# Kernel optimization log

Measured on AMD Instinct MI355X. Metric: run time of the kernel, lower is better.

Reference implementation:

```python
import jax, jax.numpy as jnp
import numpy as np

N, E, B = 10000, 100000, 64
IN_DIM, EDGE_DIM = 16, 8
HID = [32, 64]
OUT_DIM = 128
BN_EPS = 1e-5


def setup_inputs() -> dict:
    key = jax.random.key(0)
    ks = iter(jax.random.split(key, 32))
    inp = {}
    inp["x"] = jax.random.normal(next(ks), (N, IN_DIM), dtype=jnp.float32)
    inp["edge_index"] = jax.random.randint(next(ks), (2, E), 0, N, dtype=jnp.int64)
    inp["edge_attr"] = jax.random.normal(next(ks), (E, EDGE_DIM), dtype=jnp.float32)
    inp["batch"] = jnp.sort(jax.random.randint(next(ks), (N,), 0, B, dtype=jnp.int64))
    inp["edge_batch"] = jax.random.randint(next(ks), (E,), 0, B, dtype=jnp.int64)
    pre = IN_DIM
    for i, hd in enumerate(HID):
        s = 1.0 / np.sqrt(EDGE_DIM)
        inp[f"w_nn{i}"] = jax.random.uniform(next(ks), (pre * hd, EDGE_DIM), jnp.float32, -s, s)
        inp[f"b_nn{i}"] = jax.random.uniform(next(ks), (pre * hd,), jnp.float32, -s, s)
        inp[f"root{i}"] = jax.random.normal(next(ks), (pre, hd), dtype=jnp.float32) / np.sqrt(pre)
        inp[f"bias{i}"] = jnp.zeros((hd,), dtype=jnp.float32)
        inp[f"gamma{i}"] = jnp.ones((hd,), dtype=jnp.float32)
        inp[f"beta{i}"] = jnp.zeros((hd,), dtype=jnp.float32)
        pre = hd
    s = 1.0 / np.sqrt(pre)
    inp["s_w"] = jax.random.uniform(next(ks), (OUT_DIM, pre), jnp.float32, -s, s)
    inp["s_b"] = jax.random.uniform(next(ks), (OUT_DIM,), jnp.float32, -s, s)
    inp["t_w"] = jax.random.uniform(next(ks), (OUT_DIM, pre), jnp.float32, -s, s)
    inp["t_b"] = jax.random.uniform(next(ks), (OUT_DIM,), jnp.float32, -s, s)
    return inp


def _nnconv(x, edge_index, edge_attr, w_nn, b_nn, root, bias, out_dim):
    src, dst = edge_index[0], edge_index[1]
    # per-edge weight matrices [E, in_dim, out_dim]
    W = (edge_attr @ w_nn.T + b_nn).reshape(edge_attr.shape[0], -1, out_dim)
    msg = jnp.einsum('ei,eio->eo', x[src], W)  # gather + per-edge matmul
    agg = jax.ops.segment_sum(msg, dst, num_segments=N)  # scatter-add
    return agg + x @ root + bias


def _bn(x, gamma, beta):
    mu = jnp.mean(x, axis=0)
    var = jnp.mean((x - mu) ** 2, axis=0)  # biased var (torch BN training)
    return gamma * (x - mu) * jax.lax.rsqrt(var + BN_EPS) + beta


def reference(x, edge_index, edge_attr, batch, edge_batch,
              w_nn0, b_nn0, root0, bias0, gamma0, beta0,
              w_nn1, b_nn1, root1, bias1, gamma1, beta1,
              s_w, s_b, t_w, t_b):
    x = jax.nn.relu(_bn(_nnconv(x, edge_index, edge_attr, w_nn0, b_nn0, root0, bias0, HID[0]), gamma0, beta0))
    x = jax.nn.relu(_bn(_nnconv(x, edge_index, edge_attr, w_nn1, b_nn1, root1, bias1, HID[1]), gamma1, beta1))
    s_x = jnp.clip(x @ s_w.T + s_b, -30.0, 30.0)
    t_x = x @ t_w.T + t_b
    f_x = jax.nn.sigmoid(-s_x) * jnp.tanh(t_x)  # 1/(1+exp(s)) == sigmoid(-s)
    return jax.ops.segment_sum(f_x, batch, num_segments=B)
```

## Files before the change

### kernel.cpp

```cpp
#include <hip/hip_runtime.h>
#include <math.h>

#define NN 10000
#define NE 100000
#define BN_EPS 1e-5f


__device__ __forceinline__ unsigned short f2bf(float f) {
  unsigned int u = __float_as_uint(f);
  u += 0x7FFF + ((u >> 16) & 1);
  return (unsigned short)(u >> 16);
}
__device__ __forceinline__ float bf2f(unsigned short h) {
  return __uint_as_float(((unsigned int)h) << 16);
}

__global__ __launch_bounds__(256) void k_prep(
    const float* __restrict__ w0, const float* __restrict__ b0,
    const float* __restrict__ root0,
    const float* __restrict__ w1, const float* __restrict__ b1,
    const float* __restrict__ root1,
    const float* __restrict__ s_w, const float* __restrict__ t_w,
    float* __restrict__ wT0, float* __restrict__ wT1, float* __restrict__ wstT,
    float* __restrict__ st0, float* __restrict__ st1, float* __restrict__ out)
{
  int gid = blockIdx.x * 256 + threadIdx.x;
  int gsz = gridDim.x * 256;
  for (int idx = gid; idx < 16 * 320; idx += gsz) {
    int i = idx / 320, c = idx - i * 320;
    float v;
    if (c < 256)      v = w0[(i * 32 + (c & 31)) * 8 + (c >> 5)];
    else if (c < 288) v = b0[i * 32 + (c - 256)];
    else              v = root0[i * 32 + (c - 288)];
    wT0[idx] = v;
  }
  for (int idx = gid; idx < 32 * 640; idx += gsz) {
    int i = idx / 640, c = idx - i * 640;
    float v;
    if (c < 512)      v = w1[(i * 64 + (c & 63)) * 8 + (c >> 6)];
    else if (c < 576) v = b1[i * 64 + (c - 512)];
    else              v = root1[i * 64 + (c - 576)];
    wT1[idx] = v;
  }
  for (int idx = gid; idx < 64 * 256; idx += gsz) {
    int i = idx >> 8, o = idx & 255;
    wstT[idx] = (o < 128) ? s_w[o * 64 + i] : t_w[(o - 128) * 64 + i];
  }
  for (int idx = gid; idx < 64 * 128; idx += gsz) out[idx] = 0.f;
  if (gid < 64)  st0[gid] = 0.f;
  if (gid < 128) st1[gid] = 0.f;
}

__global__ __launch_bounds__(320) void k_node0(
    const float* __restrict__ x, const float* __restrict__ wT0,
    const float* __restrict__ bias0,
    unsigned short* __restrict__ G0h, float* __restrict__ h0)
{
  int c = threadIdx.x;
  float wc[16];
#pragma unroll
  for (int i = 0; i < 16; ++i) wc[i] = wT0[i * 320 + c];
  float bi = (c >= 288) ? bias0[c - 288] : 0.f;

  int n0 = blockIdx.x * 20;
  for (int n = n0; n < n0 + 20; n += 2) {
    const float4* xa = (const float4*)(x + n * 16);
    float a0 = 0.f, a1 = 0.f;
#pragma unroll
    for (int q = 0; q < 4; ++q) {
      float4 v0 = xa[q], v1 = xa[q + 4];
      a0 = fmaf(v0.x, wc[4 * q + 0], a0); a1 = fmaf(v1.x, wc[4 * q + 0], a1);
      a0 = fmaf(v0.y, wc[4 * q + 1], a0); a1 = fmaf(v1.y, wc[4 * q + 1], a1);
      a0 = fmaf(v0.z, wc[4 * q + 2], a0); a1 = fmaf(v1.z, wc[4 * q + 2], a1);
      a0 = fmaf(v0.w, wc[4 * q + 3], a0); a1 = fmaf(v1.w, wc[4 * q + 3], a1);
    }
    if (c < 288) {
      G0h[n * 288 + c]       = f2bf(a0);
      G0h[(n + 1) * 288 + c] = f2bf(a1);
    } else {
      h0[n * 32 + (c - 288)]       = a0 + bi;
      h0[(n + 1) * 32 + (c - 288)] = a1 + bi;
    }
  }
}

__global__ __launch_bounds__(256) void k_edge0(
    const int* __restrict__ ei, const float* __restrict__ ea,
    const unsigned short* __restrict__ G0h, float* __restrict__ h0)
{
  int tid = threadIdx.x;
  int slot = tid >> 5;
  int o = tid & 31;
  int stride = gridDim.x * 8;
  for (int e = blockIdx.x * 8 + slot; e < NE; e += stride) {
    int src = ei[e], dst = ei[NE + e];
    const unsigned short* gr = G0h + src * 288;
    const float* er = ea + e * 8;
    float m = bf2f(gr[256 + o]);
#pragma unroll
    for (int k = 0; k < 8; ++k) m = fmaf(er[k], bf2f(gr[k * 32 + o]), m);
    unsafeAtomicAdd(&h0[dst * 32 + o], m);
  }
}

template <int C>
__global__ __launch_bounds__(256) void k_stats(
    const float* __restrict__ h, float* __restrict__ st)
{
  const int RPB = 256 / C;
  int tid = threadIdx.x;
  int col = tid % C, rg = tid / C;
  float s1 = 0.f, s2 = 0.f;
  int step = gridDim.x * RPB;
  for (int n = blockIdx.x * RPB + rg; n < NN; n += step) {
    float v = h[n * C + col];
    s1 += v; s2 += v * v;
  }
  __shared__ float l1[256], l2[256];
  l1[tid] = s1; l2[tid] = s2;
  __syncthreads();
  if (tid < C) {
    for (int r = 1; r < RPB; ++r) { s1 += l1[r * C + tid]; s2 += l2[r * C + tid]; }
    unsafeAtomicAdd(&st[tid], s1);
    unsafeAtomicAdd(&st[C + tid], s2);
  }
}

__global__ __launch_bounds__(256) void k_x1(
    float* __restrict__ h0, const float* __restrict__ st0,
    const float* __restrict__ g0, const float* __restrict__ be0)
{
  __shared__ float sc[32], sh[32];
  int tid = threadIdx.x;
  if (tid < 32) {
    float mu  = st0[tid] * (1.0f / NN);
    float var = st0[32 + tid] * (1.0f / NN) - mu * mu;
    float s   = g0[tid] * rsqrtf(var + BN_EPS);
    sc[tid] = s;
    sh[tid] = be0[tid] - mu * s;
  }
  __syncthreads();
  const int NV = NN * 8;
  for (int i = blockIdx.x * 256 + tid; i < NV; i += gridDim.x * 256) {
    float4 v = ((const float4*)h0)[i];
    int c0 = (i * 4) & 31;
    v.x = fmaxf(fmaf(v.x, sc[c0],     sh[c0]),     0.f);
    v.y = fmaxf(fmaf(v.y, sc[c0 + 1], sh[c0 + 1]), 0.f);
    v.z = fmaxf(fmaf(v.z, sc[c0 + 2], sh[c0 + 2]), 0.f);
    v.w = fmaxf(fmaf(v.w, sc[c0 + 3], sh[c0 + 3]), 0.f);
    ((float4*)h0)[i] = v;
  }
}

__global__ __launch_bounds__(320) void k_node1(
    const float* __restrict__ x1, const float* __restrict__ wT1,
    const float* __restrict__ bias1,
    unsigned short* __restrict__ G1h, float* __restrict__ h1)
{
  int t = threadIdx.x;
  float wa[32], wb[32];
#pragma unroll
  for (int i = 0; i < 32; ++i) {
    float2 w2 = *(const float2*)(wT1 + i * 640 + 2 * t);
    wa[i] = w2.x; wb[i] = w2.y;
  }
  float bia = 0.f, bib = 0.f;
  if (t >= 288) { bia = bias1[2 * (t - 288)]; bib = bias1[2 * (t - 288) + 1]; }

  int n0 = blockIdx.x * 20;
  for (int n = n0; n < n0 + 20; n += 2) {
    const float4* xa = (const float4*)(x1 + n * 32);
    float a00 = 0.f, a01 = 0.f, a10 = 0.f, a11 = 0.f;
#pragma unroll
    for (int q = 0; q < 8; ++q) {
      float4 v0 = xa[q], v1 = xa[q + 8];
      a00 = fmaf(v0.x, wa[4 * q + 0], a00); a01 = fmaf(v0.x, wb[4 * q + 0], a01);
      a00 = fmaf(v0.y, wa[4 * q + 1], a00); a01 = fmaf(v0.y, wb[4 * q + 1], a01);
      a00 = fmaf(v0.z, wa[4 * q + 2], a00); a01 = fmaf(v0.z, wb[4 * q + 2], a01);
      a00 = fmaf(v0.w, wa[4 * q + 3], a00); a01 = fmaf(v0.w, wb[4 * q + 3], a01);
      a10 = fmaf(v1.x, wa[4 * q + 0], a10); a11 = fmaf(v1.x, wb[4 * q + 0], a11);
      a10 = fmaf(v1.y, wa[4 * q + 1], a10); a11 = fmaf(v1.y, wb[4 * q + 1], a11);
      a10 = fmaf(v1.z, wa[4 * q + 2], a10); a11 = fmaf(v1.z, wb[4 * q + 2], a11);
      a10 = fmaf(v1.w, wa[4 * q + 3], a10); a11 = fmaf(v1.w, wb[4 * q + 3], a11);
    }
    if (t < 288) {
      *(ushort2*)(G1h + n * 576 + 2 * t)       = make_ushort2(f2bf(a00), f2bf(a01));
      *(ushort2*)(G1h + (n + 1) * 576 + 2 * t) = make_ushort2(f2bf(a10), f2bf(a11));
    } else {
      int o = 2 * (t - 288);
      *(float2*)(h1 + n * 64 + o)       = make_float2(a00 + bia, a01 + bib);
      *(float2*)(h1 + (n + 1) * 64 + o) = make_float2(a10 + bia, a11 + bib);
    }
  }
}

__global__ __launch_bounds__(256) void k_edge1(
    const int* __restrict__ ei, const float* __restrict__ ea,
    const unsigned short* __restrict__ G1h, float* __restrict__ h1)
{
  int tid = threadIdx.x;
  int slot = tid >> 6;
  int o = tid & 63;
  int stride = gridDim.x * 4;
  for (int e = blockIdx.x * 4 + slot; e < NE; e += stride) {
    int src = ei[e], dst = ei[NE + e];
    const unsigned short* gr = G1h + src * 576;
    const float* er = ea + e * 8;
    float m = bf2f(gr[512 + o]);
#pragma unroll
    for (int k = 0; k < 8; ++k) m = fmaf(er[k], bf2f(gr[k * 64 + o]), m);
    unsafeAtomicAdd(&h1[dst * 64 + o], m);
  }
}

__global__ __launch_bounds__(256) void k_x2(
    float* __restrict__ h1, const float* __restrict__ st1,
    const float* __restrict__ g1, const float* __restrict__ be1)
{
  __shared__ float sc[64], sh[64];
  int tid = threadIdx.x;
  if (tid < 64) {
    float mu  = st1[tid] * (1.0f / NN);
    float var = st1[64 + tid] * (1.0f / NN) - mu * mu;
    float s   = g1[tid] * rsqrtf(var + BN_EPS);
    sc[tid] = s;
    sh[tid] = be1[tid] - mu * s;
  }
  __syncthreads();
  const int NV = NN * 16;
  for (int i = blockIdx.x * 256 + tid; i < NV; i += gridDim.x * 256) {
    float4 v = ((const float4*)h1)[i];
    int c0 = (i * 4) & 63;
    v.x = fmaxf(fmaf(v.x, sc[c0],     sh[c0]),     0.f);
    v.y = fmaxf(fmaf(v.y, sc[c0 + 1], sh[c0 + 1]), 0.f);
    v.z = fmaxf(fmaf(v.z, sc[c0 + 2], sh[c0 + 2]), 0.f);
    v.w = fmaxf(fmaf(v.w, sc[c0 + 3], sh[c0 + 3]), 0.f);
    ((float4*)h1)[i] = v;
  }
}

__global__ __launch_bounds__(256) void k_head(
    const float* __restrict__ x2, const float* __restrict__ wstT,
    const float* __restrict__ s_b, const float* __restrict__ t_b,
    const int* __restrict__ batch, float* __restrict__ out)
{
  int tid = threadIdx.x;
  int c = tid & 127, g = tid >> 7;
  int n0 = blockIdx.x * 40 + g * 20;
  int n1 = n0 + 20;
  if (n0 >= NN) return;
  if (n1 > NN) n1 = NN;

  float wsr[64], wtr[64];
#pragma unroll
  for (int k = 0; k < 64; ++k) {
    wsr[k] = wstT[k * 256 + c];
    wtr[k] = wstT[k * 256 + 128 + c];
  }
  float sb = s_b[c], tb = t_b[c];

  int bcur = batch[n0];
  float facc = 0.f;
  for (int n = n0; n < n1; ++n) {
    const float4* xr = (const float4*)(x2 + (size_t)n * 64);
    float as = 0.f, at = 0.f;
#pragma unroll
    for (int q = 0; q < 16; ++q) {
      float4 xv = xr[q];
      as = fmaf(xv.x, wsr[4 * q + 0], as); at = fmaf(xv.x, wtr[4 * q + 0], at);
      as = fmaf(xv.y, wsr[4 * q + 1], as); at = fmaf(xv.y, wtr[4 * q + 1], at);
      as = fmaf(xv.z, wsr[4 * q + 2], as); at = fmaf(xv.z, wtr[4 * q + 2], at);
      as = fmaf(xv.w, wsr[4 * q + 3], as); at = fmaf(xv.w, wtr[4 * q + 3], at);
    }
    float sv = fminf(30.f, fmaxf(-30.f, as + sb));
    float tv = at + tb;
    float f  = tanhf(tv) / (1.f + expf(sv));
    int b = batch[n];
    if (b != bcur) {
      unsafeAtomicAdd(&out[bcur * 128 + c], facc);
      bcur = b; facc = 0.f;
    }
    facc += f;
  }
  unsafeAtomicAdd(&out[bcur * 128 + c], facc);
}

extern "C" void kernel_launch(void* const* d_in, const int* in_sizes, int n_in,
                              void* d_out, int out_size, void* d_ws, size_t ws_size,
                              hipStream_t stream)
{
  const float* x     = (const float*)d_in[0];
  const int*   ei    = (const int*)d_in[1];
  const float* ea    = (const float*)d_in[2];
  const int*   batch = (const int*)d_in[3];
  const float* w0    = (const float*)d_in[5];
  const float* b0    = (const float*)d_in[6];
  const float* root0 = (const float*)d_in[7];
  const float* bias0 = (const float*)d_in[8];
  const float* g0    = (const float*)d_in[9];
  const float* be0   = (const float*)d_in[10];
  const float* w1    = (const float*)d_in[11];
  const float* b1    = (const float*)d_in[12];
  const float* root1 = (const float*)d_in[13];
  const float* bias1 = (const float*)d_in[14];
  const float* g1    = (const float*)d_in[15];
  const float* be1   = (const float*)d_in[16];
  const float* s_w   = (const float*)d_in[17];
  const float* s_b   = (const float*)d_in[18];
  const float* t_w   = (const float*)d_in[19];
  const float* t_b   = (const float*)d_in[20];
  float* out = (float*)d_out;

  float* ws   = (float*)d_ws;
  unsigned short* G0h = (unsigned short*)ws;  ws += 1440000;
  unsigned short* G1h = (unsigned short*)ws;  ws += 2880000;
  float* h0   = ws;  ws += 320000;
  float* h1   = ws;  ws += 640000;
  float* st0  = ws;  ws += 64;
  float* st1  = ws;  ws += 128;
  float* wstT = ws;  ws += 16384;
  float* wT0  = ws;  ws += 5120;
  float* wT1  = ws;  ws += 20480;

  hipLaunchKernelGGL(k_prep, dim3(64), dim3(256), 0, stream,
                     w0, b0, root0, w1, b1, root1, s_w, t_w,
                     wT0, wT1, wstT, st0, st1, out);
  hipLaunchKernelGGL(k_node0, dim3(500), dim3(320), 0, stream,
                     x, wT0, bias0, G0h, h0);
  hipLaunchKernelGGL(k_edge0, dim3(2048), dim3(256), 0, stream,
                     ei, ea, G0h, h0);
  hipLaunchKernelGGL(k_stats<32>, dim3(64), dim3(256), 0, stream, h0, st0);
  hipLaunchKernelGGL(k_x1, dim3(160), dim3(256), 0, stream, h0, st0, g0, be0);
  hipLaunchKernelGGL(k_node1, dim3(500), dim3(320), 0, stream,
                     h0, wT1, bias1, G1h, h1);
  hipLaunchKernelGGL(k_edge1, dim3(2048), dim3(256), 0, stream,
                     ei, ea, G1h, h1);
  hipLaunchKernelGGL(k_stats<64>, dim3(128), dim3(256), 0, stream, h1, st1);
  hipLaunchKernelGGL(k_x2, dim3(320), dim3(256), 0, stream, h1, st1, g1, be1);
  hipLaunchKernelGGL(k_head, dim3(250), dim3(256), 0, stream,
                     h1, wstT, s_b, t_b, batch, out);
}
```

Baseline: 203.2 us.

## Accumulate edge scatter in fp16 with packed half2 atomics

```diff
diff --git a/kernel.cpp b/kernel.cpp
--- a/kernel.cpp
+++ b/kernel.cpp
@@ -1,4 +1,5 @@
 #include <hip/hip_runtime.h>
+#include <hip/hip_fp16.h>
 #include <math.h>
 
 #define NN 10000
@@ -54,7 +55,7 @@
 __global__ __launch_bounds__(320) void k_node0(
     const float* __restrict__ x, const float* __restrict__ wT0,
     const float* __restrict__ bias0,
-    unsigned short* __restrict__ G0h, float* __restrict__ h0)
+    unsigned short* __restrict__ G0h, __half* __restrict__ h0h)
 {
   int c = threadIdx.x;
   float wc[16];
@@ -78,34 +79,39 @@
       G0h[n * 288 + c]       = f2bf(a0);
       G0h[(n + 1) * 288 + c] = f2bf(a1);
     } else {
-      h0[n * 32 + (c - 288)]       = a0 + bi;
-      h0[(n + 1) * 32 + (c - 288)] = a1 + bi;
+      h0h[n * 32 + (c - 288)]       = __float2half(a0 + bi);
+      h0h[(n + 1) * 32 + (c - 288)] = __float2half(a1 + bi);
     }
   }
 }
 
 __global__ __launch_bounds__(256) void k_edge0(
     const int* __restrict__ ei, const float* __restrict__ ea,
-    const unsigned short* __restrict__ G0h, float* __restrict__ h0)
-{
-  int tid = threadIdx.x;
-  int slot = tid >> 5;
-  int o = tid & 31;
-  int stride = gridDim.x * 8;
-  for (int e = blockIdx.x * 8 + slot; e < NE; e += stride) {
+    const unsigned short* __restrict__ G0h, __half* __restrict__ h0h)
+{
+  int tid = threadIdx.x;
+  int slot = tid >> 4;
+  int oo = (tid & 15) * 2;
+  int stride = gridDim.x * 16;
+  for (int e = blockIdx.x * 16 + slot; e < NE; e += stride) {
     int src = ei[e], dst = ei[NE + e];
     const unsigned short* gr = G0h + src * 288;
     const float* er = ea + e * 8;
-    float m = bf2f(gr[256 + o]);
-#pragma unroll
-    for (int k = 0; k < 8; ++k) m = fmaf(er[k], bf2f(gr[k * 32 + o]), m);
-    unsafeAtomicAdd(&h0[dst * 32 + o], m);
+    float m0 = bf2f(gr[256 + oo]), m1 = bf2f(gr[256 + oo + 1]);
+#pragma unroll
+    for (int k = 0; k < 8; ++k) {
+      ushort2 g2 = *(const ushort2*)(gr + k * 32 + oo);
+      float ek = er[k];
+      m0 = fmaf(ek, bf2f(g2.x), m0);
+      m1 = fmaf(ek, bf2f(g2.y), m1);
+    }
+    unsafeAtomicAdd((__half2*)(h0h + dst * 32 + oo), __floats2half2_rn(m0, m1));
   }
 }
 
 template <int C>
 __global__ __launch_bounds__(256) void k_stats(
-    const float* __restrict__ h, float* __restrict__ st)
+    const __half* __restrict__ hh, float* __restrict__ st)
 {
   const int RPB = 256 / C;
   int tid = threadIdx.x;
@@ -113,7 +119,7 @@
   float s1 = 0.f, s2 = 0.f;
   int step = gridDim.x * RPB;
   for (int n = blockIdx.x * RPB + rg; n < NN; n += step) {
-    float v = h[n * C + col];
+    float v = __half2float(hh[n * C + col]);
     s1 += v; s2 += v * v;
   }
   __shared__ float l1[256], l2[256];
@@ -127,7 +133,8 @@
 }
 
 __global__ __launch_bounds__(256) void k_x1(
-    float* __restrict__ h0, const float* __restrict__ st0,
+    const __half* __restrict__ h0h, float* __restrict__ x1,
+    const float* __restrict__ st0,
     const float* __restrict__ g0, const float* __restrict__ be0)
 {
   __shared__ float sc[32], sh[32];
@@ -140,22 +147,20 @@
     sh[tid] = be0[tid] - mu * s;
   }
   __syncthreads();
-  const int NV = NN * 8;
+  const int NV = NN * 16;
   for (int i = blockIdx.x * 256 + tid; i < NV; i += gridDim.x * 256) {
-    float4 v = ((const float4*)h0)[i];
-    int c0 = (i * 4) & 31;
-    v.x = fmaxf(fmaf(v.x, sc[c0],     sh[c0]),     0.f);
-    v.y = fmaxf(fmaf(v.y, sc[c0 + 1], sh[c0 + 1]), 0.f);
-    v.z = fmaxf(fmaf(v.z, sc[c0 + 2], sh[c0 + 2]), 0.f);
-    v.w = fmaxf(fmaf(v.w, sc[c0 + 3], sh[c0 + 3]), 0.f);
-    ((float4*)h0)[i] = v;
+    __half2 hv = ((const __half2*)h0h)[i];
+    int c0 = (i * 2) & 31;
+    float vx = fmaxf(fmaf(__half2float(hv.x), sc[c0],     sh[c0]),     0.f);
+    float vy = fmaxf(fmaf(__half2float(hv.y), sc[c0 + 1], sh[c0 + 1]), 0.f);
+    ((float2*)x1)[i] = make_float2(vx, vy);
   }
 }
 
 __global__ __launch_bounds__(320) void k_node1(
     const float* __restrict__ x1, const float* __restrict__ wT1,
     const float* __restrict__ bias1,
-    unsigned short* __restrict__ G1h, float* __restrict__ h1)
+    unsigned short* __restrict__ G1h, __half* __restrict__ h1h)
 {
   int t = threadIdx.x;
   float wa[32], wb[32];
@@ -188,33 +193,39 @@
       *(ushort2*)(G1h + (n + 1) * 576 + 2 * t) = make_ushort2(f2bf(a10), f2bf(a11));
     } else {
       int o = 2 * (t - 288);
-      *(float2*)(h1 + n * 64 + o)       = make_float2(a00 + bia, a01 + bib);
-      *(float2*)(h1 + (n + 1) * 64 + o) = make_float2(a10 + bia, a11 + bib);
+      *(__half2*)(h1h + n * 64 + o)       = __floats2half2_rn(a00 + bia, a01 + bib);
+      *(__half2*)(h1h + (n + 1) * 64 + o) = __floats2half2_rn(a10 + bia, a11 + bib);
     }
   }
 }
 
 __global__ __launch_bounds__(256) void k_edge1(
     const int* __restrict__ ei, const float* __restrict__ ea,
-    const unsigned short* __restrict__ G1h, float* __restrict__ h1)
-{
-  int tid = threadIdx.x;
-  int slot = tid >> 6;
-  int o = tid & 63;
-  int stride = gridDim.x * 4;
-  for (int e = blockIdx.x * 4 + slot; e < NE; e += stride) {
+    const unsigned short* __restrict__ G1h, __half* __restrict__ h1h)
+{
+  int tid = threadIdx.x;
+  int slot = tid >> 5;
+  int oo = (tid & 31) * 2;
+  int stride = gridDim.x * 8;
+  for (int e = blockIdx.x * 8 + slot; e < NE; e += stride) {
     int src = ei[e], dst = ei[NE + e];
     const unsigned short* gr = G1h + src * 576;
     const float* er = ea + e * 8;
-    float m = bf2f(gr[512 + o]);
-#pragma unroll
-    for (int k = 0; k < 8; ++k) m = fmaf(er[k], bf2f(gr[k * 64 + o]), m);
-    unsafeAtomicAdd(&h1[dst * 64 + o], m);
+    float m0 = bf2f(gr[512 + oo]), m1 = bf2f(gr[512 + oo + 1]);
+#pragma unroll
+    for (int k = 0; k < 8; ++k) {
+      ushort2 g2 = *(const ushort2*)(gr + k * 64 + oo);
+      float ek = er[k];
+      m0 = fmaf(ek, bf2f(g2.x), m0);
+      m1 = fmaf(ek, bf2f(g2.y), m1);
+    }
+    unsafeAtomicAdd((__half2*)(h1h + dst * 64 + oo), __floats2half2_rn(m0, m1));
   }
 }
 
 __global__ __launch_bounds__(256) void k_x2(
-    float* __restrict__ h1, const float* __restrict__ st1,
+    const __half* __restrict__ h1h, float* __restrict__ x2,
+    const float* __restrict__ st1,
     const float* __restrict__ g1, const float* __restrict__ be1)
 {
   __shared__ float sc[64], sh[64];
@@ -227,15 +238,13 @@
     sh[tid] = be1[tid] - mu * s;
   }
   __syncthreads();
-  const int NV = NN * 16;
+  const int NV = NN * 32;
   for (int i = blockIdx.x * 256 + tid; i < NV; i += gridDim.x * 256) {
-    float4 v = ((const float4*)h1)[i];
-    int c0 = (i * 4) & 63;
-    v.x = fmaxf(fmaf(v.x, sc[c0],     sh[c0]),     0.f);
-    v.y = fmaxf(fmaf(v.y, sc[c0 + 1], sh[c0 + 1]), 0.f);
-    v.z = fmaxf(fmaf(v.z, sc[c0 + 2], sh[c0 + 2]), 0.f);
-    v.w = fmaxf(fmaf(v.w, sc[c0 + 3], sh[c0 + 3]), 0.f);
-    ((float4*)h1)[i] = v;
+    __half2 hv = ((const __half2*)h1h)[i];
+    int c0 = (i * 2) & 63;
+    float vx = fmaxf(fmaf(__half2float(hv.x), sc[c0],     sh[c0]),     0.f);
+    float vy = fmaxf(fmaf(__half2float(hv.y), sc[c0 + 1], sh[c0 + 1]), 0.f);
+    ((float2*)x2)[i] = make_float2(vx, vy);
   }
 }
 
@@ -314,8 +323,10 @@
   float* ws   = (float*)d_ws;
   unsigned short* G0h = (unsigned short*)ws;  ws += 1440000;
   unsigned short* G1h = (unsigned short*)ws;  ws += 2880000;
-  float* h0   = ws;  ws += 320000;
-  float* h1   = ws;  ws += 640000;
+  __half* h0h = (__half*)ws;  ws += 160000;
+  __half* h1h = (__half*)ws;  ws += 320000;
+  float* x1   = ws;  ws += 320000;
+  float* x2   = ws;  ws += 640000;
   float* st0  = ws;  ws += 64;
   float* st1  = ws;  ws += 128;
   float* wstT = ws;  ws += 16384;
@@ -326,17 +337,17 @@
                      w0, b0, root0, w1, b1, root1, s_w, t_w,
                      wT0, wT1, wstT, st0, st1, out);
   hipLaunchKernelGGL(k_node0, dim3(500), dim3(320), 0, stream,
-                     x, wT0, bias0, G0h, h0);
+                     x, wT0, bias0, G0h, h0h);
   hipLaunchKernelGGL(k_edge0, dim3(2048), dim3(256), 0, stream,
-                     ei, ea, G0h, h0);
-  hipLaunchKernelGGL(k_stats<32>, dim3(64), dim3(256), 0, stream, h0, st0);
-  hipLaunchKernelGGL(k_x1, dim3(160), dim3(256), 0, stream, h0, st0, g0, be0);
+                     ei, ea, G0h, h0h);
+  hipLaunchKernelGGL(k_stats<32>, dim3(64), dim3(256), 0, stream, h0h, st0);
+  hipLaunchKernelGGL(k_x1, dim3(160), dim3(256), 0, stream, h0h, x1, st0, g0, be0);
   hipLaunchKernelGGL(k_node1, dim3(500), dim3(320), 0, stream,
-                     h0, wT1, bias1, G1h, h1);
+                     x1, wT1, bias1, G1h, h1h);
   hipLaunchKernelGGL(k_edge1, dim3(2048), dim3(256), 0, stream,
-                     ei, ea, G1h, h1);
-  hipLaunchKernelGGL(k_stats<64>, dim3(128), dim3(256), 0, stream, h1, st1);
-  hipLaunchKernelGGL(k_x2, dim3(320), dim3(256), 0, stream, h1, st1, g1, be1);
+                     ei, ea, G1h, h1h);
+  hipLaunchKernelGGL(k_stats<64>, dim3(128), dim3(256), 0, stream, h1h, st1);
+  hipLaunchKernelGGL(k_x2, dim3(320), dim3(256), 0, stream, h1h, x2, st1, g1, be1);
   hipLaunchKernelGGL(k_head, dim3(250), dim3(256), 0, stream,
-                     h1, wstT, s_b, t_b, batch, out);
-}
+                     x2, wstT, s_b, t_b, batch, out);
+}
```

Result: faster. 191.2 us (-5.9%).
